# Kernel optimization log

Measured on AMD Instinct MI355X. Metric: run time of the kernel, lower is better.

## Reference

```python
import jax, jax.numpy as jnp
import numpy as np

H = 256  # hidden_dim


def _mlp(x, w1, b1, w2, b2):
    # Linear -> ReLU -> (Dropout=identity in eval) -> Linear
    return jax.nn.relu(x @ w1 + b1) @ w2 + b2


def setup_inputs() -> dict:
    key = jax.random.key(0)
    ks = jax.random.split(key, 9)
    bsz, seq = 32, 4096
    s = 1.0 / np.sqrt(2 * H)
    inp = {
        "h": jax.random.normal(ks[0], (bsz, seq, H), dtype=jnp.float32),
        "mask": jnp.ones((bsz, seq), dtype=jnp.float32),
        "ew1": jax.random.uniform(ks[1], (2 * H, H), minval=-s, maxval=s),
        "eb1": jax.random.uniform(ks[2], (H,), minval=-s, maxval=s),
        "ew2": jax.random.uniform(ks[3], (H, H), minval=-s, maxval=s),
        "eb2": jax.random.uniform(ks[4], (H,), minval=-s, maxval=s),
        "nw1": jax.random.uniform(ks[5], (2 * H, H), minval=-s, maxval=s),
        "nb1": jax.random.uniform(ks[6], (H,), minval=-s, maxval=s),
        "nw2": jax.random.uniform(ks[7], (H, H), minval=-s, maxval=s),
        "nb2": jax.random.uniform(ks[8], (H,), minval=-s, maxval=s),
    }
    return inp


def reference(h, mask, ew1, eb1, ew2, eb2, nw1, nb1, nw2, nb2):
    left = h[:, :-1, :]   # [B, S-1, H]
    right = h[:, 1:, :]   # [B, S-1, H]
    m_lr = _mlp(jnp.concatenate([left, right], axis=-1), ew1, eb1, ew2, eb2)
    m_rl = _mlp(jnp.concatenate([right, left], axis=-1), ew1, eb1, ew2, eb2)
    # shifted scatter-add: agg[:,1:] += m_lr ; agg[:,:-1] += m_rl
    zcol = jnp.zeros_like(h[:, :1, :])
    agg = jnp.concatenate([zcol, m_lr], axis=1) + jnp.concatenate([m_rl, zcol], axis=1)
    updated = _mlp(jnp.concatenate([h, agg], axis=-1), nw1, nb1, nw2, nb2)
    updated = updated * mask[:, :, None]
    return h + updated
```

## Files before the change

kernel.cpp:

```cpp
#include <hip/hip_runtime.h>
#include <hip/hip_bf16.h>

typedef __bf16 bf16_t;
typedef bf16_t bf16x8 __attribute__((ext_vector_type(8)));
typedef bf16_t bf16x4 __attribute__((ext_vector_type(4)));
typedef float f32x4 __attribute__((ext_vector_type(4)));

#define SEQ 4096
#define BSZ 32
#define T_TOK 64
#define PROWS 66
#define LSTR 264

#define OFF_HBF 0
#define OFF_A   (PROWS * LSTR)
#define OFF_B   (2 * PROWS * LSTR)
#define SMEM_ELEMS (3 * PROWS * LSTR)
#define SMEM_BYTES (SMEM_ELEMS * 2)

#define W1F 0
#define NAF 131072
#define W2F 196608
#define NBF 262144
#define N2F 327680
#define WS_ELEMS 393216

#define BAR() asm volatile("s_waitcnt lgkmcnt(0)\n\ts_barrier" ::: "memory")

__global__ void wprep(const float* __restrict__ ew1, const float* __restrict__ ew2,
                      const float* __restrict__ nw1, const float* __restrict__ nw2,
                      bf16_t* __restrict__ wsw) {
    int idx = blockIdx.x * 256 + threadIdx.x;
    int frag = idx >> 9, o = idx & 511;
    int l = o >> 3, e = o & 7;
    int r = l & 15, kg = l >> 4;
    float v;
    if (frag < 256) {
        int nt = frag >> 3, ks = frag & 7;
        int k = ks * 32 + kg * 8 + e;
        int n = nt * 16 + r;
        v = (nt < 16) ? ew1[k * 256 + n] : ew1[(256 + k) * 256 + (n - 256)];
    } else {
        int f = frag - 256;
        int m = f >> 7;
        int fl = f & 127;
        int nt = fl >> 3, ks = fl & 7;
        int k = ks * 32 + kg * 8 + e;
        int n = nt * 16 + r;
        const float* src = (m == 0) ? (nw1 + k * 256)
                         : (m == 1) ? (ew2 + k * 256)
                         : (m == 2) ? (nw1 + (256 + k) * 256)
                         :            (nw2 + k * 256);
        v = src[n];
    }
    wsw[idx] = (bf16_t)v;
}

#define WFRAG(base, nt, ks) \
    (*(const bf16x8*)(wsw + (base) + (((nt) * 8 + (ks)) << 9) + (lane << 3)))
#define AFRAG(off, rbase, ks) \
    (*(const bf16x8*)(sm + (off) + ((rbase) + c) * LSTR + (kg << 3) + ((ks) << 5)))

__launch_bounds__(512, 2)
__global__ void gnl_kernel(const float* __restrict__ h, const float* __restrict__ mask,
                           const float* __restrict__ eb1, const float* __restrict__ eb2,
                           const float* __restrict__ nb1, const float* __restrict__ nb2,
                           const bf16_t* __restrict__ wsw, float* __restrict__ out) {
    extern __shared__ bf16_t sm[];

    const int tid   = threadIdx.x;
    const int lane  = tid & 63;
    const int w     = tid >> 6;
    const int batch = blockIdx.x >> 6;
    const int tile  = blockIdx.x & 63;
    const int t0    = tile * T_TOK;
    const long baseTok = (long)batch * SEQ;

    const int c   = lane & 15;
    const int kg  = lane >> 4;
    const int crb = kg << 2;

    const int n0a = w * 16;
    const int n0b = (w + 8) * 16;

    for (int cc = tid; cc < PROWS * 32; cc += 512) {
        int r = cc >> 5;
        int fc = (cc & 31) << 3;
        int t = t0 - 1 + r;
        bf16x8 vals;
        if (t >= 0 && t < SEQ) {
            const float* src = h + (((long)(baseTok + t)) << 8) + fc;
            float4 x0 = ((const float4*)src)[0];
            float4 x1 = ((const float4*)src)[1];
            vals[0] = (bf16_t)x0.x; vals[1] = (bf16_t)x0.y;
            vals[2] = (bf16_t)x0.z; vals[3] = (bf16_t)x0.w;
            vals[4] = (bf16_t)x1.x; vals[5] = (bf16_t)x1.y;
            vals[6] = (bf16_t)x1.z; vals[7] = (bf16_t)x1.w;
        } else {
#pragma unroll
            for (int j = 0; j < 8; ++j) vals[j] = (bf16_t)0.0f;
        }
        *(bf16x8*)(sm + OFF_HBF + r * LSTR + fc) = vals;
    }
    BAR();

#pragma unroll
    for (int p = 0; p < 2; ++p) {
        bf16x8 wa[8], wb[8];
#pragma unroll
        for (int ks = 0; ks < 8; ++ks) {
            wa[ks] = WFRAG(W1F, w + p * 16, ks);
            wb[ks] = WFRAG(W1F, w + p * 16 + 8, ks);
        }
        int poff = p ? OFF_B : OFF_A;
#pragma unroll
        for (int mt = 0; mt < 5; ++mt) {
            bf16x8 hf[8];
#pragma unroll
            for (int ks = 0; ks < 8; ++ks) hf[ks] = AFRAG(OFF_HBF, mt * 16, ks);
            f32x4 aA = {0.f, 0.f, 0.f, 0.f}, aB = {0.f, 0.f, 0.f, 0.f};
            __builtin_amdgcn_s_setprio(1);
#pragma unroll
            for (int ks = 0; ks < 8; ++ks)
                aA = __builtin_amdgcn_mfma_f32_16x16x32_bf16(wa[ks], hf[ks], aA, 0, 0, 0);
#pragma unroll
            for (int ks = 0; ks < 8; ++ks)
                aB = __builtin_amdgcn_mfma_f32_16x16x32_bf16(wb[ks], hf[ks], aB, 0, 0, 0);
            __builtin_amdgcn_s_setprio(0);
            int row = mt * 16 + c;
            if (row < PROWS) {
                bf16x4 pA, pB;
#pragma unroll
                for (int j = 0; j < 4; ++j) { pA[j] = (bf16_t)aA[j]; pB[j] = (bf16_t)aB[j]; }
                *(bf16x4*)(sm + poff + row * LSTR + n0a + crb) = pA;
                *(bf16x4*)(sm + poff + row * LSTR + n0b + crb) = pB;
            }
        }
    }

    f32x4 ha[4][2];
    {
        bf16x8 na[8], nb8[8];
#pragma unroll
        for (int ks = 0; ks < 8; ++ks) {
            na[ks]  = WFRAG(NAF, w, ks);
            nb8[ks] = WFRAG(NAF, w + 8, ks);
        }
#pragma unroll
        for (int tm = 0; tm < 4; ++tm) {
            bf16x8 hf[8];
#pragma unroll
            for (int ks = 0; ks < 8; ++ks) hf[ks] = AFRAG(OFF_HBF, 1 + tm * 16, ks);
            f32x4 a0 = {0.f, 0.f, 0.f, 0.f}, a1 = {0.f, 0.f, 0.f, 0.f};
            __builtin_amdgcn_s_setprio(1);
#pragma unroll
            for (int ks = 0; ks < 8; ++ks)
                a0 = __builtin_amdgcn_mfma_f32_16x16x32_bf16(na[ks], hf[ks], a0, 0, 0, 0);
#pragma unroll
            for (int ks = 0; ks < 8; ++ks)
                a1 = __builtin_amdgcn_mfma_f32_16x16x32_bf16(nb8[ks], hf[ks], a1, 0, 0, 0);
            __builtin_amdgcn_s_setprio(0);
            ha[tm][0] = a0; ha[tm][1] = a1;
        }
    }

    bf16x8 w2a[8], w2b[8];
#pragma unroll
    for (int ks = 0; ks < 8; ++ks) {
        w2a[ks] = WFRAG(W2F, w, ks);
        w2b[ks] = WFRAG(W2F, w + 8, ks);
    }
    BAR();

#pragma unroll
    for (int it = 0; it < 4; ++it) {
        int cc = tid + it * 512;
        int i = cc >> 5;
        int fc = (cc & 31) << 3;
        float bl = (t0 + i >= 1) ? 1.f : 0.f;
        float br = (t0 + i <= SEQ - 2) ? 1.f : 0.f;
        bf16x8 aL = *(const bf16x8*)(sm + OFF_A + i * LSTR + fc);
        bf16x8 aR = *(const bf16x8*)(sm + OFF_A + (i + 2) * LSTR + fc);
        bf16x8 bC = *(const bf16x8*)(sm + OFF_B + (i + 1) * LSTR + fc);
        float4 b1a = *(const float4*)(eb1 + fc);
        float4 b1b = *(const float4*)(eb1 + fc + 4);
        bf16x8 sv;
#pragma unroll
        for (int j = 0; j < 8; ++j) {
            float b1f = (j < 4) ? ((const float*)&b1a)[j] : ((const float*)&b1b)[j - 4];
            float x = (float)bC[j] + b1f;
            float l = fmaxf((float)aL[j] + x, 0.f) * bl;
            float r = fmaxf((float)aR[j] + x, 0.f) * br;
            sv[j] = (bf16_t)(l + r);
        }
        *(bf16x8*)(sm + OFF_HBF + i * LSTR + fc) = sv;
    }
    BAR();

    {
        float4 b2a = *(const float4*)(eb2 + n0a + crb);
        float4 b2b = *(const float4*)(eb2 + n0b + crb);
#pragma unroll
        for (int mt = 0; mt < 4; ++mt) {
            bf16x8 sf[8];
#pragma unroll
            for (int ks = 0; ks < 8; ++ks) sf[ks] = AFRAG(OFF_HBF, mt * 16, ks);
            f32x4 g0 = {0.f, 0.f, 0.f, 0.f}, g1 = {0.f, 0.f, 0.f, 0.f};
            __builtin_amdgcn_s_setprio(1);
#pragma unroll
            for (int ks = 0; ks < 8; ++ks)
                g0 = __builtin_amdgcn_mfma_f32_16x16x32_bf16(w2a[ks], sf[ks], g0, 0, 0, 0);
#pragma unroll
            for (int ks = 0; ks < 8; ++ks)
                g1 = __builtin_amdgcn_mfma_f32_16x16x32_bf16(w2b[ks], sf[ks], g1, 0, 0, 0);
            __builtin_amdgcn_s_setprio(0);
            int i = mt * 16 + c;
            float cnt = ((t0 + i >= 1) ? 1.f : 0.f) + ((t0 + i <= SEQ - 2) ? 1.f : 0.f);
            bf16x4 p0, p1;
#pragma unroll
            for (int j = 0; j < 4; ++j) {
                p0[j] = (bf16_t)(g0[j] + cnt * ((const float*)&b2a)[j]);
                p1[j] = (bf16_t)(g1[j] + cnt * ((const float*)&b2b)[j]);
            }
            *(bf16x4*)(sm + OFF_A + i * LSTR + n0a + crb) = p0;
            *(bf16x4*)(sm + OFF_A + i * LSTR + n0b + crb) = p1;
        }
    }
    bf16x8 nba[8], nbb[8];
#pragma unroll
    for (int ks = 0; ks < 8; ++ks) {
        nba[ks] = WFRAG(NBF, w, ks);
        nbb[ks] = WFRAG(NBF, w + 8, ks);
    }
    BAR();

    {
        float4 n1a = *(const float4*)(nb1 + n0a + crb);
        float4 n1b = *(const float4*)(nb1 + n0b + crb);
#pragma unroll
        for (int tm = 0; tm < 4; ++tm) {
            bf16x8 gf[8];
#pragma unroll
            for (int ks = 0; ks < 8; ++ks) gf[ks] = AFRAG(OFF_A, tm * 16, ks);
            f32x4 a0 = ha[tm][0], a1 = ha[tm][1];
            __builtin_amdgcn_s_setprio(1);
#pragma unroll
            for (int ks = 0; ks < 8; ++ks)
                a0 = __builtin_amdgcn_mfma_f32_16x16x32_bf16(nba[ks], gf[ks], a0, 0, 0, 0);
#pragma unroll
            for (int ks = 0; ks < 8; ++ks)
                a1 = __builtin_amdgcn_mfma_f32_16x16x32_bf16(nbb[ks], gf[ks], a1, 0, 0, 0);
            __builtin_amdgcn_s_setprio(0);
            bf16x4 p0, p1;
#pragma unroll
            for (int j = 0; j < 4; ++j) {
                p0[j] = (bf16_t)fmaxf(a0[j] + ((const float*)&n1a)[j], 0.f);
                p1[j] = (bf16_t)fmaxf(a1[j] + ((const float*)&n1b)[j], 0.f);
            }
            int i = tm * 16 + c;
            *(bf16x4*)(sm + OFF_B + i * LSTR + n0a + crb) = p0;
            *(bf16x4*)(sm + OFF_B + i * LSTR + n0b + crb) = p1;
        }
    }
    bf16x8 n2a[8], n2b[8];
#pragma unroll
    for (int ks = 0; ks < 8; ++ks) {
        n2a[ks] = WFRAG(N2F, w, ks);
        n2b[ks] = WFRAG(N2F, w + 8, ks);
    }
    BAR();

    {
        float4 v2a = *(const float4*)(nb2 + n0a + crb);
        float4 v2b = *(const float4*)(nb2 + n0b + crb);
#pragma unroll
        for (int tm = 0; tm < 4; ++tm) {
            bf16x8 hnf[8];
#pragma unroll
            for (int ks = 0; ks < 8; ++ks) hnf[ks] = AFRAG(OFF_B, tm * 16, ks);
            f32x4 a0 = {0.f, 0.f, 0.f, 0.f}, a1 = {0.f, 0.f, 0.f, 0.f};
            __builtin_amdgcn_s_setprio(1);
#pragma unroll
            for (int ks = 0; ks < 8; ++ks)
                a0 = __builtin_amdgcn_mfma_f32_16x16x32_bf16(n2a[ks], hnf[ks], a0, 0, 0, 0);
#pragma unroll
            for (int ks = 0; ks < 8; ++ks)
                a1 = __builtin_amdgcn_mfma_f32_16x16x32_bf16(n2b[ks], hnf[ks], a1, 0, 0, 0);
            __builtin_amdgcn_s_setprio(0);
            long t = baseTok + t0 + tm * 16 + c;
            float m = mask[t];
            long g0 = (t << 8) + n0a + crb;
            long g1 = (t << 8) + n0b + crb;
            float4 h0 = *(const float4*)(h + g0);
            float4 h1 = *(const float4*)(h + g1);
            float4 o0, o1;
            o0.x = h0.x + m * (a0[0] + v2a.x);
            o0.y = h0.y + m * (a0[1] + v2a.y);
            o0.z = h0.z + m * (a0[2] + v2a.z);
            o0.w = h0.w + m * (a0[3] + v2a.w);
            o1.x = h1.x + m * (a1[0] + v2b.x);
            o1.y = h1.y + m * (a1[1] + v2b.y);
            o1.z = h1.z + m * (a1[2] + v2b.z);
            o1.w = h1.w + m * (a1[3] + v2b.w);
            *(float4*)(out + g0) = o0;
            *(float4*)(out + g1) = o1;
        }
    }
}

extern "C" void kernel_launch(void* const* d_in, const int* in_sizes, int n_in,
                              void* d_out, int out_size, void* d_ws, size_t ws_size,
                              hipStream_t stream) {
    const float* h    = (const float*)d_in[0];
    const float* mask = (const float*)d_in[1];
    const float* ew1  = (const float*)d_in[2];
    const float* eb1  = (const float*)d_in[3];
    const float* ew2  = (const float*)d_in[4];
    const float* eb2  = (const float*)d_in[5];
    const float* nw1  = (const float*)d_in[6];
    const float* nb1  = (const float*)d_in[7];
    const float* nw2  = (const float*)d_in[8];
    const float* nb2  = (const float*)d_in[9];
    float* out   = (float*)d_out;
    bf16_t* wsw  = (bf16_t*)d_ws;

    wprep<<<WS_ELEMS / 256, 256, 0, stream>>>(ew1, ew2, nw1, nw2, wsw);

    hipFuncSetAttribute(reinterpret_cast<const void*>(gnl_kernel),
                        hipFuncAttributeMaxDynamicSharedMemorySize, SMEM_BYTES);

    gnl_kernel<<<BSZ * (SEQ / T_TOK), 512, SMEM_BYTES, stream>>>(
        h, mask, eb1, eb2, nb1, nb2, wsw, out);
}
```

Measured before the change: 171.2 us.

## Fold edge second-layer weight into node first-layer weight, double-buffer LDS fragments

Precomputes ew2 @ nw1[256:] and eb2 @ nw1[256:] in a new prep kernel. This removes a whole 64x256x256 GEMM stage per tile, its barrier and an LDS round-trip in the main kernel; the edge bias is applied as cnt * folded bias. LDS fragment loads are also double-buffered so the next tile's A fragments load while the current MFMAs run, and each ks step now interleaves the two MFMA chains. In exchange it adds a small naive prep GEMM kernel and changes rounding, since the aggregated message is no longer materialized in bf16.

```diff
diff --git a/kernel.cpp b/kernel.cpp
--- a/kernel.cpp
+++ b/kernel.cpp
@@ -12,59 +12,66 @@
 #define PROWS 66
 #define LSTR 264
 
-#define OFF_HBF 0
-#define OFF_A   (PROWS * LSTR)
-#define OFF_B   (2 * PROWS * LSTR)
+#define OFF_P0 0
+#define OFF_P1 (PROWS * LSTR)
+#define OFF_P2 (2 * PROWS * LSTR)
 #define SMEM_ELEMS (3 * PROWS * LSTR)
 #define SMEM_BYTES (SMEM_ELEMS * 2)
 
 #define W1F 0
 #define NAF 131072
-#define W2F 196608
-#define NBF 262144
-#define N2F 327680
-#define WS_ELEMS 393216
+#define WBF 196608
+#define N2F 262144
+#define B2N 327680
 
 #define BAR() asm volatile("s_waitcnt lgkmcnt(0)\n\ts_barrier" ::: "memory")
 
-__global__ void wprep(const float* __restrict__ ew1, const float* __restrict__ ew2,
-                      const float* __restrict__ nw1, const float* __restrict__ nw2,
-                      bf16_t* __restrict__ wsw) {
+__global__ void wprep(const float* __restrict__ ew1, const float* __restrict__ nw1,
+                      const float* __restrict__ nw2, bf16_t* __restrict__ wsw) {
     int idx = blockIdx.x * 256 + threadIdx.x;
-    int frag = idx >> 9, o = idx & 511;
+    int region, rel, outbase;
+    if (idx < 131072)      { region = 0; rel = idx;          outbase = W1F; }
+    else if (idx < 196608) { region = 1; rel = idx - 131072; outbase = NAF; }
+    else                   { region = 2; rel = idx - 196608; outbase = N2F; }
+    int f = rel >> 9, o = rel & 511;
     int l = o >> 3, e = o & 7;
     int r = l & 15, kg = l >> 4;
+    int nt = f >> 3, ks = f & 7;
+    int k = ks * 32 + kg * 8 + e;
+    int n = nt * 16 + r;
     float v;
-    if (frag < 256) {
-        int nt = frag >> 3, ks = frag & 7;
-        int k = ks * 32 + kg * 8 + e;
-        int n = nt * 16 + r;
+    if (region == 0)
         v = (nt < 16) ? ew1[k * 256 + n] : ew1[(256 + k) * 256 + (n - 256)];
+    else if (region == 1)
+        v = nw1[k * 256 + n];
+    else
+        v = nw2[k * 256 + n];
+    wsw[outbase + rel] = (bf16_t)v;
+}
+
+__global__ void wprep2(const float* __restrict__ ew2, const float* __restrict__ eb2,
+                       const float* __restrict__ nw1, bf16_t* __restrict__ wsw) {
+    int k = blockIdx.x;
+    int n = threadIdx.x;
+    if (k < 256) {
+        float acc = 0.f;
+        for (int j = 0; j < 256; ++j)
+            acc += ew2[k * 256 + j] * nw1[(256 + j) * 256 + n];
+        int ks = k >> 5, kg = (k >> 3) & 3, e = k & 7;
+        int nt = n >> 4, r = n & 15;
+        wsw[WBF + ((nt * 8 + ks) << 9) + ((kg * 16 + r) << 3) + e] = (bf16_t)acc;
     } else {
-        int f = frag - 256;
-        int m = f >> 7;
-        int fl = f & 127;
-        int nt = fl >> 3, ks = fl & 7;
-        int k = ks * 32 + kg * 8 + e;
-        int n = nt * 16 + r;
-        const float* src = (m == 0) ? (nw1 + k * 256)
-                         : (m == 1) ? (ew2 + k * 256)
-                         : (m == 2) ? (nw1 + (256 + k) * 256)
-                         :            (nw2 + k * 256);
-        v = src[n];
-    }
-    wsw[idx] = (bf16_t)v;
-}
-
-#define WFRAG(base, nt, ks) \
-    (*(const bf16x8*)(wsw + (base) + (((nt) * 8 + (ks)) << 9) + (lane << 3)))
-#define AFRAG(off, rbase, ks) \
-    (*(const bf16x8*)(sm + (off) + ((rbase) + c) * LSTR + (kg << 3) + ((ks) << 5)))
+        float acc = 0.f;
+        for (int j = 0; j < 256; ++j)
+            acc += eb2[j] * nw1[(256 + j) * 256 + n];
+        ((float*)(wsw + B2N))[n] = acc;
+    }
+}
 
 __launch_bounds__(512, 2)
 __global__ void gnl_kernel(const float* __restrict__ h, const float* __restrict__ mask,
-                           const float* __restrict__ eb1, const float* __restrict__ eb2,
-                           const float* __restrict__ nb1, const float* __restrict__ nb2,
+                           const float* __restrict__ eb1, const float* __restrict__ nb1,
+                           const float* __restrict__ nb2,
                            const bf16_t* __restrict__ wsw, float* __restrict__ out) {
     extern __shared__ bf16_t sm[];
 
@@ -79,9 +86,29 @@
     const int c   = lane & 15;
     const int kg  = lane >> 4;
     const int crb = kg << 2;
-
     const int n0a = w * 16;
     const int n0b = (w + 8) * 16;
+
+    auto loadw = [&](bf16x8 (&f)[8], int base, int nt) {
+#pragma unroll
+        for (int ks = 0; ks < 8; ++ks)
+            f[ks] = *(const bf16x8*)(wsw + base + ((nt * 8 + ks) << 9) + (lane << 3));
+    };
+    auto loada = [&](bf16x8 (&f)[8], int poff, int rbase) {
+        const bf16_t* p = sm + poff + (rbase + c) * LSTR + (kg << 3);
+#pragma unroll
+        for (int ks = 0; ks < 8; ++ks) f[ks] = *(const bf16x8*)(p + (ks << 5));
+    };
+    auto mfma2 = [&](bf16x8 (&f)[8], bf16x8 (&wa)[8], bf16x8 (&wb)[8],
+                     f32x4& a0, f32x4& a1) {
+        __builtin_amdgcn_s_setprio(1);
+#pragma unroll
+        for (int ks = 0; ks < 8; ++ks) {
+            a0 = __builtin_amdgcn_mfma_f32_16x16x32_bf16(wa[ks], f[ks], a0, 0, 0, 0);
+            a1 = __builtin_amdgcn_mfma_f32_16x16x32_bf16(wb[ks], f[ks], a1, 0, 0, 0);
+        }
+        __builtin_amdgcn_s_setprio(0);
+    };
 
     for (int cc = tid; cc < PROWS * 32; cc += 512) {
         int r = cc >> 5;
@@ -100,33 +127,25 @@
 #pragma unroll
             for (int j = 0; j < 8; ++j) vals[j] = (bf16_t)0.0f;
         }
-        *(bf16x8*)(sm + OFF_HBF + r * LSTR + fc) = vals;
+        *(bf16x8*)(sm + OFF_P0 + r * LSTR + fc) = vals;
     }
     BAR();
 
 #pragma unroll
     for (int p = 0; p < 2; ++p) {
         bf16x8 wa[8], wb[8];
-#pragma unroll
-        for (int ks = 0; ks < 8; ++ks) {
-            wa[ks] = WFRAG(W1F, w + p * 16, ks);
-            wb[ks] = WFRAG(W1F, w + p * 16 + 8, ks);
-        }
-        int poff = p ? OFF_B : OFF_A;
+        loadw(wa, W1F, w + p * 16);
+        loadw(wb, W1F, w + p * 16 + 8);
+        int poff = p ? OFF_P2 : OFF_P1;
+        bf16x8 fA[8], fB[8];
+        loada(fA, OFF_P0, 0);
 #pragma unroll
         for (int mt = 0; mt < 5; ++mt) {
-            bf16x8 hf[8];
-#pragma unroll
-            for (int ks = 0; ks < 8; ++ks) hf[ks] = AFRAG(OFF_HBF, mt * 16, ks);
+            bf16x8 (&cur)[8] = (mt & 1) ? fB : fA;
+            bf16x8 (&nxt)[8] = (mt & 1) ? fA : fB;
+            if (mt < 4) loada(nxt, OFF_P0, (mt + 1) * 16);
             f32x4 aA = {0.f, 0.f, 0.f, 0.f}, aB = {0.f, 0.f, 0.f, 0.f};
-            __builtin_amdgcn_s_setprio(1);
-#pragma unroll
-            for (int ks = 0; ks < 8; ++ks)
-                aA = __builtin_amdgcn_mfma_f32_16x16x32_bf16(wa[ks], hf[ks], aA, 0, 0, 0);
-#pragma unroll
-            for (int ks = 0; ks < 8; ++ks)
-                aB = __builtin_amdgcn_mfma_f32_16x16x32_bf16(wb[ks], hf[ks], aB, 0, 0, 0);
-            __builtin_amdgcn_s_setprio(0);
+            mfma2(cur, wa, wb, aA, aB);
             int row = mt * 16 + c;
             if (row < PROWS) {
                 bf16x4 pA, pB;
@@ -141,35 +160,24 @@
     f32x4 ha[4][2];
     {
         bf16x8 na[8], nb8[8];
-#pragma unroll
-        for (int ks = 0; ks < 8; ++ks) {
-            na[ks]  = WFRAG(NAF, w, ks);
-            nb8[ks] = WFRAG(NAF, w + 8, ks);
-        }
+        loadw(na, NAF, w);
+        loadw(nb8, NAF, w + 8);
+        bf16x8 fA[8], fB[8];
+        loada(fA, OFF_P0, 1);
 #pragma unroll
         for (int tm = 0; tm < 4; ++tm) {
-            bf16x8 hf[8];
-#pragma unroll
-            for (int ks = 0; ks < 8; ++ks) hf[ks] = AFRAG(OFF_HBF, 1 + tm * 16, ks);
+            bf16x8 (&cur)[8] = (tm & 1) ? fB : fA;
+            bf16x8 (&nxt)[8] = (tm & 1) ? fA : fB;
+            if (tm < 3) loada(nxt, OFF_P0, tm * 16 + 17);
             f32x4 a0 = {0.f, 0.f, 0.f, 0.f}, a1 = {0.f, 0.f, 0.f, 0.f};
-            __builtin_amdgcn_s_setprio(1);
-#pragma unroll
-            for (int ks = 0; ks < 8; ++ks)
-                a0 = __builtin_amdgcn_mfma_f32_16x16x32_bf16(na[ks], hf[ks], a0, 0, 0, 0);
-#pragma unroll
-            for (int ks = 0; ks < 8; ++ks)
-                a1 = __builtin_amdgcn_mfma_f32_16x16x32_bf16(nb8[ks], hf[ks], a1, 0, 0, 0);
-            __builtin_amdgcn_s_setprio(0);
+            mfma2(cur, na, nb8, a0, a1);
             ha[tm][0] = a0; ha[tm][1] = a1;
         }
     }
 
-    bf16x8 w2a[8], w2b[8];
-#pragma unroll
-    for (int ks = 0; ks < 8; ++ks) {
-        w2a[ks] = WFRAG(W2F, w, ks);
-        w2b[ks] = WFRAG(W2F, w + 8, ks);
-    }
+    bf16x8 wba[8], wbb[8];
+    loadw(wba, WBF, w);
+    loadw(wbb, WBF, w + 8);
     BAR();
 
 #pragma unroll
@@ -179,9 +187,9 @@
         int fc = (cc & 31) << 3;
         float bl = (t0 + i >= 1) ? 1.f : 0.f;
         float br = (t0 + i <= SEQ - 2) ? 1.f : 0.f;
-        bf16x8 aL = *(const bf16x8*)(sm + OFF_A + i * LSTR + fc);
-        bf16x8 aR = *(const bf16x8*)(sm + OFF_A + (i + 2) * LSTR + fc);
-        bf16x8 bC = *(const bf16x8*)(sm + OFF_B + (i + 1) * LSTR + fc);
+        bf16x8 aL = *(const bf16x8*)(sm + OFF_P1 + i * LSTR + fc);
+        bf16x8 aR = *(const bf16x8*)(sm + OFF_P1 + (i + 2) * LSTR + fc);
+        bf16x8 bC = *(const bf16x8*)(sm + OFF_P2 + (i + 1) * LSTR + fc);
         float4 b1a = *(const float4*)(eb1 + fc);
         float4 b1b = *(const float4*)(eb1 + fc + 4);
         bf16x8 sv;
@@ -193,106 +201,61 @@
             float r = fmaxf((float)aR[j] + x, 0.f) * br;
             sv[j] = (bf16_t)(l + r);
         }
-        *(bf16x8*)(sm + OFF_HBF + i * LSTR + fc) = sv;
-    }
-    BAR();
-
-    {
-        float4 b2a = *(const float4*)(eb2 + n0a + crb);
-        float4 b2b = *(const float4*)(eb2 + n0b + crb);
-#pragma unroll
-        for (int mt = 0; mt < 4; ++mt) {
-            bf16x8 sf[8];
-#pragma unroll
-            for (int ks = 0; ks < 8; ++ks) sf[ks] = AFRAG(OFF_HBF, mt * 16, ks);
-            f32x4 g0 = {0.f, 0.f, 0.f, 0.f}, g1 = {0.f, 0.f, 0.f, 0.f};
-            __builtin_amdgcn_s_setprio(1);
-#pragma unroll
-            for (int ks = 0; ks < 8; ++ks)
-                g0 = __builtin_amdgcn_mfma_f32_16x16x32_bf16(w2a[ks], sf[ks], g0, 0, 0, 0);
-#pragma unroll
-            for (int ks = 0; ks < 8; ++ks)
-                g1 = __builtin_amdgcn_mfma_f32_16x16x32_bf16(w2b[ks], sf[ks], g1, 0, 0, 0);
-            __builtin_amdgcn_s_setprio(0);
-            int i = mt * 16 + c;
-            float cnt = ((t0 + i >= 1) ? 1.f : 0.f) + ((t0 + i <= SEQ - 2) ? 1.f : 0.f);
-            bf16x4 p0, p1;
-#pragma unroll
-            for (int j = 0; j < 4; ++j) {
-                p0[j] = (bf16_t)(g0[j] + cnt * ((const float*)&b2a)[j]);
-                p1[j] = (bf16_t)(g1[j] + cnt * ((const float*)&b2b)[j]);
-            }
-            *(bf16x4*)(sm + OFF_A + i * LSTR + n0a + crb) = p0;
-            *(bf16x4*)(sm + OFF_A + i * LSTR + n0b + crb) = p1;
-        }
-    }
-    bf16x8 nba[8], nbb[8];
-#pragma unroll
-    for (int ks = 0; ks < 8; ++ks) {
-        nba[ks] = WFRAG(NBF, w, ks);
-        nbb[ks] = WFRAG(NBF, w + 8, ks);
+        *(bf16x8*)(sm + OFF_P0 + i * LSTR + fc) = sv;
     }
     BAR();
 
     {
         float4 n1a = *(const float4*)(nb1 + n0a + crb);
         float4 n1b = *(const float4*)(nb1 + n0b + crb);
+        const float* b2n = (const float*)(wsw + B2N);
+        float4 c2a = *(const float4*)(b2n + n0a + crb);
+        float4 c2b = *(const float4*)(b2n + n0b + crb);
+        bf16x8 fA[8], fB[8];
+        loada(fA, OFF_P0, 0);
 #pragma unroll
         for (int tm = 0; tm < 4; ++tm) {
-            bf16x8 gf[8];
-#pragma unroll
-            for (int ks = 0; ks < 8; ++ks) gf[ks] = AFRAG(OFF_A, tm * 16, ks);
+            bf16x8 (&cur)[8] = (tm & 1) ? fB : fA;
+            bf16x8 (&nxt)[8] = (tm & 1) ? fA : fB;
+            if (tm < 3) loada(nxt, OFF_P0, (tm + 1) * 16);
             f32x4 a0 = ha[tm][0], a1 = ha[tm][1];
-            __builtin_amdgcn_s_setprio(1);
-#pragma unroll
-            for (int ks = 0; ks < 8; ++ks)
-                a0 = __builtin_amdgcn_mfma_f32_16x16x32_bf16(nba[ks], gf[ks], a0, 0, 0, 0);
-#pragma unroll
-            for (int ks = 0; ks < 8; ++ks)
-                a1 = __builtin_amdgcn_mfma_f32_16x16x32_bf16(nbb[ks], gf[ks], a1, 0, 0, 0);
-            __builtin_amdgcn_s_setprio(0);
+            mfma2(cur, wba, wbb, a0, a1);
+            int row = tm * 16 + c;
+            int t = t0 + row;
+            float cnt = ((t >= 1) ? 1.f : 0.f) + ((t <= SEQ - 2) ? 1.f : 0.f);
             bf16x4 p0, p1;
 #pragma unroll
             for (int j = 0; j < 4; ++j) {
-                p0[j] = (bf16_t)fmaxf(a0[j] + ((const float*)&n1a)[j], 0.f);
-                p1[j] = (bf16_t)fmaxf(a1[j] + ((const float*)&n1b)[j], 0.f);
+                p0[j] = (bf16_t)fmaxf(a0[j] + ((const float*)&n1a)[j] + cnt * ((const float*)&c2a)[j], 0.f);
+                p1[j] = (bf16_t)fmaxf(a1[j] + ((const float*)&n1b)[j] + cnt * ((const float*)&c2b)[j], 0.f);
             }
-            int i = tm * 16 + c;
-            *(bf16x4*)(sm + OFF_B + i * LSTR + n0a + crb) = p0;
-            *(bf16x4*)(sm + OFF_B + i * LSTR + n0b + crb) = p1;
+            *(bf16x4*)(sm + OFF_P1 + row * LSTR + n0a + crb) = p0;
+            *(bf16x4*)(sm + OFF_P1 + row * LSTR + n0b + crb) = p1;
         }
     }
     bf16x8 n2a[8], n2b[8];
-#pragma unroll
-    for (int ks = 0; ks < 8; ++ks) {
-        n2a[ks] = WFRAG(N2F, w, ks);
-        n2b[ks] = WFRAG(N2F, w + 8, ks);
-    }
+    loadw(n2a, N2F, w);
+    loadw(n2b, N2F, w + 8);
     BAR();
 
     {
         float4 v2a = *(const float4*)(nb2 + n0a + crb);
         float4 v2b = *(const float4*)(nb2 + n0b + crb);
+        bf16x8 fA[8], fB[8];
+        loada(fA, OFF_P1, 0);
 #pragma unroll
         for (int tm = 0; tm < 4; ++tm) {
-            bf16x8 hnf[8];
-#pragma unroll
-            for (int ks = 0; ks < 8; ++ks) hnf[ks] = AFRAG(OFF_B, tm * 16, ks);
-            f32x4 a0 = {0.f, 0.f, 0.f, 0.f}, a1 = {0.f, 0.f, 0.f, 0.f};
-            __builtin_amdgcn_s_setprio(1);
-#pragma unroll
-            for (int ks = 0; ks < 8; ++ks)
-                a0 = __builtin_amdgcn_mfma_f32_16x16x32_bf16(n2a[ks], hnf[ks], a0, 0, 0, 0);
-#pragma unroll
-            for (int ks = 0; ks < 8; ++ks)
-                a1 = __builtin_amdgcn_mfma_f32_16x16x32_bf16(n2b[ks], hnf[ks], a1, 0, 0, 0);
-            __builtin_amdgcn_s_setprio(0);
             long t = baseTok + t0 + tm * 16 + c;
             float m = mask[t];
             long g0 = (t << 8) + n0a + crb;
             long g1 = (t << 8) + n0b + crb;
             float4 h0 = *(const float4*)(h + g0);
             float4 h1 = *(const float4*)(h + g1);
+            bf16x8 (&cur)[8] = (tm & 1) ? fB : fA;
+            bf16x8 (&nxt)[8] = (tm & 1) ? fA : fB;
+            if (tm < 3) loada(nxt, OFF_P1, (tm + 1) * 16);
+            f32x4 a0 = {0.f, 0.f, 0.f, 0.f}, a1 = {0.f, 0.f, 0.f, 0.f};
+            mfma2(cur, n2a, n2b, a0, a1);
             float4 o0, o1;
             o0.x = h0.x + m * (a0[0] + v2a.x);
             o0.y = h0.y + m * (a0[1] + v2a.y);
@@ -324,11 +287,12 @@
     float* out   = (float*)d_out;
     bf16_t* wsw  = (bf16_t*)d_ws;
 
-    wprep<<<WS_ELEMS / 256, 256, 0, stream>>>(ew1, ew2, nw1, nw2, wsw);
+    wprep<<<1024, 256, 0, stream>>>(ew1, nw1, nw2, wsw);
+    wprep2<<<257, 256, 0, stream>>>(ew2, eb2, nw1, wsw);
 
     hipFuncSetAttribute(reinterpret_cast<const void*>(gnl_kernel),
                         hipFuncAttributeMaxDynamicSharedMemorySize, SMEM_BYTES);
 
     gnl_kernel<<<BSZ * (SEQ / T_TOK), 512, SMEM_BYTES, stream>>>(
-        h, mask, eb1, eb2, nb1, nb2, wsw, out);
-}
+        h, mask, eb1, nb1, nb2, wsw, out);
+}
```

New measurement: 169.5 us. Within noise of the previous version (-1.0%).
